# Kernel optimization log

Hardware: AMD Instinct MI355X
Metric: run time of the kernel (lower is better)

Reference implementation:

```python
import jax, jax.numpy as jnp
import numpy as np

B, T, I, O, A = 64, 512, 1024, 1024, 3


def setup_inputs() -> dict:
    key = jax.random.key(0)
    ks = jax.random.split(key, 10)
    stdv = 1.0 / np.sqrt(O)
    u = lambda k, shape: jax.random.uniform(k, shape, jnp.float32, -stdv, stdv)
    return dict(
        x=jax.random.normal(ks[0], (B, T, I), jnp.float32),
        ww_x=u(ks[1], (O, I)), ww_y=u(ks[2], (O, O)), bw=u(ks[3], (O,)),
        wb_x=u(ks[4], (O, I)), wb_y=u(ks[5], (O, O)), bb=u(ks[6], (O,)),
        wa_x=u(ks[7], (A, I)), wa_y=u(ks[8], (A, O)), ba=u(ks[9], (A,)),
    )


def _asnn_forward(x, ww_x, ww_y, bw, wb_x, wb_y, bb, wa_x, wa_y, ba):
    b_, t_, _ = x.shape
    o_ = ww_x.shape[0]
    # Precompute all input projections once (time-major for scan): [T,B,O] / [T,B,A]
    xw = jnp.einsum('bti,oi->tbo', x, ww_x) + bw
    xb = jnp.einsum('bti,oi->tbo', x, wb_x) + bb
    xa = jnp.einsum('bti,ai->tba', x, wa_x) + ba

    def step(carry, inp):
        y, h = carry  # [B,O], [B,O]
        xw_t, xb_t, xa_t = inp
        w = jax.nn.sigmoid(xw_t + h @ ww_y.T)
        b = jnp.tanh(xb_t + h @ wb_y.T)
        wa = jax.nn.sigmoid(xa_t + h @ wa_y.T)  # [B,A]
        y = w * y + b
        # original uses in-place F.leaky_relu_, so the carried y is leaky-relu'd
        y = jnp.where(y >= 0, y, 0.01 * y)
        hcat = jnp.stack([y, jnp.tanh(y), jax.nn.softplus(y)], axis=-1)  # [B,O,3]
        h = jnp.tanh(jnp.einsum('boa,ba->bo', hcat, wa) / 10.0)
        return (y, h), h

    init = (jnp.zeros((b_, o_), x.dtype), jnp.zeros((b_, o_), x.dtype))
    (y_fin, _), hs = jax.lax.scan(step, init, (xw, xb, xa))
    out = jnp.transpose(hs, (1, 0, 2))  # [B,T,O]
    return out, y_fin


def reference(x, ww_x, ww_y, bw, wb_x, wb_y, bb, wa_x, wa_y, ba):
    return _asnn_forward(x, ww_x, ww_y, bw, wb_x, wb_y, bb, wa_x, wa_y, ba)
```

## Files before the change

kernel.cpp:

```cpp
#include <hip/hip_runtime.h>
#include <hip/hip_fp16.h>


#define B_ 64
#define T_ 512
#define I_ 1024
#define O_ 1024

typedef __attribute__((ext_vector_type(8))) _Float16 half8;
typedef __attribute__((ext_vector_type(4))) float f32x4;
typedef __attribute__((ext_vector_type(4))) float float4v;
typedef __attribute__((ext_vector_type(4))) unsigned int uint4v;

__device__ __forceinline__ float sigm_f(float x) { return 1.f / (1.f + __expf(-x)); }
__device__ __forceinline__ float tanh_f(float x) { return 1.f - 2.f / (1.f + __expf(2.f * x)); }

#define WS_XW    0
#define WS_W1    134217728
#define WS_W2P   134217728
#define WS_XA    139460608
#define WS_HBUF  139853824
#define HBUF_BYTES 524288

__global__ void init_w1(const float* __restrict__ ww_x, const float* __restrict__ wb_x,
                        _Float16* __restrict__ W1) {
    const int total = 2048 * 1024;
    for (int idx = blockIdx.x * blockDim.x + threadIdx.x; idx < total;
         idx += gridDim.x * blockDim.x) {
        int n = idx >> 10, i = idx & 1023;
        float v = (n < 1024) ? ww_x[n * 1024 + i] : wb_x[(n - 1024) * 1024 + i];
        W1[idx] = (_Float16)v;
    }
}

__global__ void init_w2p(const float* __restrict__ ww_y, const float* __restrict__ wb_y,
                         const float* __restrict__ wa_y, _Float16* __restrict__ W2P) {
    const int total = 32 * 4 * 5 * 8 * 64 * 8;
    for (int idx = blockIdx.x * blockDim.x + threadIdx.x; idx < total;
         idx += gridDim.x * blockDim.x) {
        int j = idx & 7;
        int lane = (idx >> 3) & 63;
        int ktl = (idx >> 9) & 7;
        int rest = idx >> 12;
        int tile = rest % 5;
        int gw = rest / 5;
        int w = gw & 3, g = gw >> 2;
        int frow = lane & 15, fch = lane >> 4;
        int r = tile * 16 + frow;
        int k = w * 256 + ktl * 32 + fch * 8 + j;
        float v = 0.f;
        if (r < 32)      v = ww_y[(g * 32 + r) * 1024 + k];
        else if (r < 64) v = wb_y[(g * 32 + r - 32) * 1024 + k];
        else if (r < 67) v = wa_y[(r - 64) * 1024 + k];
        W2P[idx] = (_Float16)v;
    }
}

__global__ __launch_bounds__(256) void gemm1(const float* __restrict__ x,
                                             const _Float16* __restrict__ W1,
                                             const float* __restrict__ bw,
                                             const float* __restrict__ bb,
                                             _Float16* __restrict__ XW) {
    __shared__ _Float16 At[2][128][40];
    __shared__ _Float16 Bt[2][128][40];
    const int tid = threadIdx.x;
    const int lane = tid & 63, wid = tid >> 6;
    const int wr = wid >> 1, wc = wid & 1;
    const int ntile = blockIdx.x & 15;
    const int mtile = blockIdx.x >> 4;
    const long m0 = (long)mtile * 128;
    const int n0 = ntile * 128;

    const int r = tid >> 1, hf = tid & 1;
    const int bidx = (int)((m0 + r) & 63);
    const int tt = (int)((m0 + r) >> 6);
    const float* xrow = x + ((size_t)bidx * T_ + tt) * I_ + hf * 16;
    const _Float16* brow = W1 + (size_t)(n0 + r) * 1024 + hf * 16;

    float4v av[4];
    uint4v bv[2];
    auto stage_regs = [&](int kt) {
        const float4v* pa = (const float4v*)(xrow + kt * 32);
        av[0] = pa[0]; av[1] = pa[1]; av[2] = pa[2]; av[3] = pa[3];
        const uint4v* pb = (const uint4v*)(brow + kt * 32);
        bv[0] = pb[0]; bv[1] = pb[1];
    };
    auto write_lds = [&](int buf) {
        union { _Float16 h[16]; half8 v[2]; } u;
        #pragma unroll
        for (int q = 0; q < 4; ++q)
            #pragma unroll
            for (int c = 0; c < 4; ++c) u.h[q * 4 + c] = (_Float16)av[q][c];
        half8* dA = (half8*)&At[buf][r][hf * 16];
        dA[0] = u.v[0]; dA[1] = u.v[1];
        uint4v* dB = (uint4v*)&Bt[buf][r][hf * 16];
        dB[0] = bv[0]; dB[1] = bv[1];
    };

    f32x4 acc[4][4];
    #pragma unroll
    for (int i = 0; i < 4; ++i)
        #pragma unroll
        for (int j = 0; j < 4; ++j) acc[i][j] = (f32x4){0.f, 0.f, 0.f, 0.f};

    const int frow = lane & 15, fch = lane >> 4;
    auto compute = [&](int buf) {
        half8 a[4], b[4];
        #pragma unroll
        for (int i = 0; i < 4; ++i)
            a[i] = *(const half8*)&At[buf][wr * 64 + i * 16 + frow][fch * 8];
        #pragma unroll
        for (int j = 0; j < 4; ++j)
            b[j] = *(const half8*)&Bt[buf][wc * 64 + j * 16 + frow][fch * 8];
        #pragma unroll
        for (int i = 0; i < 4; ++i)
            #pragma unroll
            for (int j = 0; j < 4; ++j)
                acc[i][j] = __builtin_amdgcn_mfma_f32_16x16x32_f16(a[i], b[j], acc[i][j], 0, 0, 0);
    };

    stage_regs(0);
    write_lds(0);
    __syncthreads();
    for (int kt = 0; kt < 32; ++kt) {
        const int cur = kt & 1;
        if (kt < 31) stage_regs(kt + 1);
        compute(cur);
        if (kt < 31) { write_lds(cur ^ 1); __syncthreads(); }
    }

    const int orow = (lane >> 4) * 4, ocol = lane & 15;
    #pragma unroll
    for (int j = 0; j < 4; ++j) {
        const int n = n0 + wc * 64 + j * 16 + ocol;
        const float bias = (n < 1024) ? bw[n] : bb[n - 1024];
        #pragma unroll
        for (int i = 0; i < 4; ++i) {
            const long mb = m0 + wr * 64 + i * 16 + orow;
            #pragma unroll
            for (int rr = 0; rr < 4; ++rr)
                XW[(size_t)(mb + rr) * 2048 + n] = (_Float16)(acc[i][j][rr] + bias);
        }
    }
}

__global__ __launch_bounds__(256) void xa_proj(const float* __restrict__ x,
                                               const float* __restrict__ wa_x,
                                               const float* __restrict__ ba,
                                               float* __restrict__ XA) {
    const int wid = threadIdx.x >> 6, lane = threadIdx.x & 63;
    const long m = (long)blockIdx.x * 4 + wid;
    const int b = (int)(m & 63), t = (int)(m >> 6);
    const float4v* xr = (const float4v*)(x + ((size_t)b * T_ + t) * I_);
    const float4v* w0 = (const float4v*)(wa_x);
    const float4v* w1 = (const float4v*)(wa_x + 1024);
    const float4v* w2 = (const float4v*)(wa_x + 2048);
    float a0 = 0.f, a1 = 0.f, a2 = 0.f;
    #pragma unroll
    for (int j = 0; j < 4; ++j) {
        const int idx = j * 64 + lane;
        float4v xv = xr[idx];
        float4v v0 = w0[idx], v1 = w1[idx], v2 = w2[idx];
        a0 += xv[0] * v0[0] + xv[1] * v0[1] + xv[2] * v0[2] + xv[3] * v0[3];
        a1 += xv[0] * v1[0] + xv[1] * v1[1] + xv[2] * v1[2] + xv[3] * v1[3];
        a2 += xv[0] * v2[0] + xv[1] * v2[1] + xv[2] * v2[2] + xv[3] * v2[3];
    }
    #pragma unroll
    for (int mset = 32; mset >= 1; mset >>= 1) {
        a0 += __shfl_xor(a0, mset);
        a1 += __shfl_xor(a1, mset);
        a2 += __shfl_xor(a2, mset);
    }
    if (lane == 0) {
        XA[m * 3 + 0] = a0 + ba[0];
        XA[m * 3 + 1] = a1 + ba[1];
        XA[m * 3 + 2] = a2 + ba[2];
    }
}

#define XOR4(v) ((v[0] ^ tg) | (v[1] ^ tg) | (v[2] ^ tg) | (v[3] ^ tg))
#define PK2(lo, hi) (((lo) >> 16) | ((hi) & 0xffff0000u))
#define PACKF(dst, A, Bv) { union { unsigned u[4]; half8 h; } uu; \
    uu.u[0] = PK2(A[0], A[1]); uu.u[1] = PK2(A[2], A[3]); \
    uu.u[2] = PK2(Bv[0], Bv[1]); uu.u[3] = PK2(Bv[2], Bv[3]); dst = uu.h; }

__global__ __launch_bounds__(256, 1) void scan_kernel(
    const _Float16* __restrict__ XW, const float* __restrict__ XA,
    const _Float16* __restrict__ W2P,
    float* __restrict__ out, float* __restrict__ yfin,
    unsigned int* __restrict__ Hbuf) {
    __shared__ __align__(16) float PR[2][4][5][16][12];

    const int tid = threadIdx.x;
    const int lane = tid & 63, w = tid >> 6;
    const int d = blockIdx.x & 7, g = blockIdx.x >> 3;
    const int b0 = d * 8, n0 = g * 32;
    const int bl = tid >> 5;
    const int nn = tid & 31;
    const int frow = lane & 15, fch = lane >> 4;
    const int hi = lane >> 4, col = lane & 15;

    half8 Bf[5][8];
    {
        const _Float16* wp = W2P + ((size_t)(g * 4 + w) * 40 * 64 + lane) * 8;
        #pragma unroll
        for (int tile = 0; tile < 5; ++tile)
            #pragma unroll
            for (int ktl = 0; ktl < 8; ++ktl)
                Bf[tile][ktl] = *(const half8*)(wp + (size_t)(tile * 8 + ktl) * 512);
    }

    float y = 0.f;
    for (int t = 0; t < T_; ++t) {
        const int par = t & 1;
        f32x4 acc[5];
        #pragma unroll
        for (int tile = 0; tile < 5; ++tile) acc[tile] = (f32x4){0.f, 0.f, 0.f, 0.f};

        if (t > 0) {
            half8 af[8];
            #pragma unroll
            for (int f = 0; f < 8; ++f) af[f] = (half8)(_Float16)0.f;

            if (frow < 8) {
                const unsigned tg = (unsigned)t;
                const unsigned* hp = Hbuf + ((size_t)((t - 1) & 1) * 64 + b0 + frow) * 1024
                                     + w * 256 + fch * 8;
                uint4v q0, q1, q2, q3, q4, q5, q6, q7, q8, q9, q10, q11, q12, q13, q14, q15;
                while (true) {
                    asm volatile(
                        "global_load_dwordx4 %0, %8, off sc0 sc1\n\t"
                        "global_load_dwordx4 %1, %8, off offset:16 sc0 sc1\n\t"
                        "global_load_dwordx4 %2, %8, off offset:128 sc0 sc1\n\t"
                        "global_load_dwordx4 %3, %8, off offset:144 sc0 sc1\n\t"
                        "global_load_dwordx4 %4, %8, off offset:256 sc0 sc1\n\t"
                        "global_load_dwordx4 %5, %8, off offset:272 sc0 sc1\n\t"
                        "global_load_dwordx4 %6, %8, off offset:384 sc0 sc1\n\t"
                        "global_load_dwordx4 %7, %8, off offset:400 sc0 sc1"
                        : "=&v"(q0), "=&v"(q1), "=&v"(q2), "=&v"(q3),
                          "=&v"(q4), "=&v"(q5), "=&v"(q6), "=&v"(q7)
                        : "v"(hp) : "memory");
                    asm volatile(
                        "global_load_dwordx4 %0, %8, off offset:512 sc0 sc1\n\t"
                        "global_load_dwordx4 %1, %8, off offset:528 sc0 sc1\n\t"
                        "global_load_dwordx4 %2, %8, off offset:640 sc0 sc1\n\t"
                        "global_load_dwordx4 %3, %8, off offset:656 sc0 sc1\n\t"
                        "global_load_dwordx4 %4, %8, off offset:768 sc0 sc1\n\t"
                        "global_load_dwordx4 %5, %8, off offset:784 sc0 sc1\n\t"
                        "global_load_dwordx4 %6, %8, off offset:896 sc0 sc1\n\t"
                        "global_load_dwordx4 %7, %8, off offset:912 sc0 sc1\n\t"
                        "s_waitcnt vmcnt(0)"
                        : "=&v"(q8), "=&v"(q9), "=&v"(q10), "=&v"(q11),
                          "=&v"(q12), "=&v"(q13), "=&v"(q14), "=&v"(q15)
                        : "v"(hp) : "memory");
                    unsigned bad = (XOR4(q0) | XOR4(q1) | XOR4(q2) | XOR4(q3)
                                  | XOR4(q4) | XOR4(q5) | XOR4(q6) | XOR4(q7)
                                  | XOR4(q8) | XOR4(q9) | XOR4(q10) | XOR4(q11)
                                  | XOR4(q12) | XOR4(q13) | XOR4(q14) | XOR4(q15)) & 0xffffu;
                    if (!__any((int)bad)) break;
                }
                PACKF(af[0], q0, q1);   PACKF(af[1], q2, q3);
                PACKF(af[2], q4, q5);   PACKF(af[3], q6, q7);
                PACKF(af[4], q8, q9);   PACKF(af[5], q10, q11);
                PACKF(af[6], q12, q13); PACKF(af[7], q14, q15);
            }
            #pragma unroll
            for (int f = 0; f < 8; ++f)
                #pragma unroll
                for (int tile = 0; tile < 5; ++tile)
                    acc[tile] = __builtin_amdgcn_mfma_f32_16x16x32_f16(af[f], Bf[tile][f],
                                                                       acc[tile], 0, 0, 0);
        }

        const size_t mrow = (size_t)t * 64 + (size_t)(b0 + bl);
        const float xwv = (float)XW[mrow * 2048 + (n0 + nn)];
        const float xbv = (float)XW[mrow * 2048 + 1024 + (n0 + nn)];
        const float xa0 = XA[mrow * 3 + 0];
        const float xa1 = XA[mrow * 3 + 1];
        const float xa2 = XA[mrow * 3 + 2];

        if (t > 0 && hi < 2) {
            #pragma unroll
            for (int tile = 0; tile < 5; ++tile)
                *(f32x4*)&PR[par][w][tile][col][hi * 4] = acc[tile];
        }
        __syncthreads();

        float gw = 0.f, gb = 0.f, pav = 0.f;
        if (t > 0) {
            const int tw = nn >> 4, c = nn & 15, ac = nn & 3;
            #pragma unroll
            for (int ww = 0; ww < 4; ++ww) {
                gw += PR[par][ww][tw][c][bl];
                gb += PR[par][ww][2 + tw][c][bl];
                pav += PR[par][ww][4][ac][bl];
            }
        }
        const float pa0 = __shfl(pav, (lane & 32) + 0);
        const float pa1 = __shfl(pav, (lane & 32) + 1);
        const float pa2 = __shfl(pav, (lane & 32) + 2);

        const float wv = sigm_f(xwv + gw);
        const float bgt = tanh_f(xbv + gb);
        const float wa0 = sigm_f(xa0 + pa0);
        const float wa1 = sigm_f(xa1 + pa1);
        const float wa2 = sigm_f(xa2 + pa2);
        y = wv * y + bgt;
        y = (y >= 0.f) ? y : 0.01f * y;
        const float th = tanh_f(y);
        const float sp = (y > 20.f) ? y : __logf(1.f + __expf(y));
        const float h = tanh_f(0.1f * (y * wa0 + th * wa1 + sp * wa2));

        _Float16 hh = (_Float16)h;
        const unsigned hu = ((unsigned)*(unsigned short*)&hh << 16) | (unsigned)(t + 1);
        __hip_atomic_store(&Hbuf[((size_t)par * 64 + b0 + bl) * 1024 + n0 + nn], hu,
                           __ATOMIC_RELAXED, __HIP_MEMORY_SCOPE_AGENT);
        out[((size_t)(b0 + bl) * T_ + t) * O_ + n0 + nn] = h;
    }
    yfin[(size_t)(b0 + bl) * O_ + n0 + nn] = y;
}

extern "C" void kernel_launch(void* const* d_in, const int* in_sizes, int n_in,
                              void* d_out, int out_size, void* d_ws, size_t ws_size,
                              hipStream_t stream) {
    const float* x    = (const float*)d_in[0];
    const float* ww_x = (const float*)d_in[1];
    const float* ww_y = (const float*)d_in[2];
    const float* bw   = (const float*)d_in[3];
    const float* wb_x = (const float*)d_in[4];
    const float* wb_y = (const float*)d_in[5];
    const float* bb   = (const float*)d_in[6];
    const float* wa_x = (const float*)d_in[7];
    const float* wa_y = (const float*)d_in[8];
    const float* ba   = (const float*)d_in[9];

    char* ws = (char*)d_ws;
    _Float16* XW  = (_Float16*)(ws + WS_XW);
    _Float16* W1  = (_Float16*)(ws + WS_W1);
    _Float16* W2P = (_Float16*)(ws + WS_W2P);
    float* XA = (float*)(ws + WS_XA);
    unsigned int* Hbuf = (unsigned int*)(ws + WS_HBUF);

    float* out = (float*)d_out;
    float* yfin = out + (size_t)B_ * T_ * O_;

    hipMemsetAsync(Hbuf, 0, HBUF_BYTES, stream);
    hipLaunchKernelGGL(init_w1, dim3(2048), dim3(256), 0, stream, ww_x, wb_x, W1);
    hipLaunchKernelGGL(gemm1, dim3(4096), dim3(256), 0, stream, x, W1, bw, bb, XW);
    hipLaunchKernelGGL(init_w2p, dim3(1024), dim3(256), 0, stream, ww_y, wb_y, wa_y, W2P);
    hipLaunchKernelGGL(xa_proj, dim3(8192), dim3(256), 0, stream, x, wa_x, ba, XA);
    hipLaunchKernelGGL(scan_kernel, dim3(256), dim3(256), 0, stream,
                       XW, XA, W2P, out, yfin, Hbuf);
}
```

Before: 2.253 ms.

## Replace per-element tagged handoff with packed fp16 h buffer plus per-wave flags

The inter-block hidden-state exchange stops tagging every fp16 value with a 16-bit timestep inside a 32-bit word. h is now packed two halves per word, and each wave publishes a separate per-step flag after a vmcnt wait. Consumers spin on 128 flags for their batch group and then read half as many bytes of h. The XW/XA gate inputs for the next step are also prefetched into registers during the current step. The risks are extra flag-poll latency plus a store-then-flag ordering that depends on a waitcnt rather than a release fence.

```diff
diff --git a/kernel.cpp b/kernel.cpp
--- a/kernel.cpp
+++ b/kernel.cpp
@@ -11,16 +11,21 @@
 typedef __attribute__((ext_vector_type(4))) float f32x4;
 typedef __attribute__((ext_vector_type(4))) float float4v;
 typedef __attribute__((ext_vector_type(4))) unsigned int uint4v;
+typedef __attribute__((ext_vector_type(2))) unsigned int uint2v;
 
 __device__ __forceinline__ float sigm_f(float x) { return 1.f / (1.f + __expf(-x)); }
 __device__ __forceinline__ float tanh_f(float x) { return 1.f - 2.f / (1.f + __expf(2.f * x)); }
+__device__ __forceinline__ float h2f_bits(unsigned short u) {
+    union { unsigned short s; _Float16 h; } x; x.s = u; return (float)x.h;
+}
 
 #define WS_XW    0
 #define WS_W1    134217728
 #define WS_W2P   134217728
 #define WS_XA    139460608
 #define WS_HBUF  139853824
-#define HBUF_BYTES 524288
+#define WS_FLG   140115968
+#define FLG_BYTES 8192
 
 __global__ void init_w1(const float* __restrict__ ww_x, const float* __restrict__ wb_x,
                         _Float16* __restrict__ W1) {
@@ -178,17 +183,11 @@
     }
 }
 
-#define XOR4(v) ((v[0] ^ tg) | (v[1] ^ tg) | (v[2] ^ tg) | (v[3] ^ tg))
-#define PK2(lo, hi) (((lo) >> 16) | ((hi) & 0xffff0000u))
-#define PACKF(dst, A, Bv) { union { unsigned u[4]; half8 h; } uu; \
-    uu.u[0] = PK2(A[0], A[1]); uu.u[1] = PK2(A[2], A[3]); \
-    uu.u[2] = PK2(Bv[0], Bv[1]); uu.u[3] = PK2(Bv[2], Bv[3]); dst = uu.h; }
-
 __global__ __launch_bounds__(256, 1) void scan_kernel(
     const _Float16* __restrict__ XW, const float* __restrict__ XA,
     const _Float16* __restrict__ W2P,
     float* __restrict__ out, float* __restrict__ yfin,
-    unsigned int* __restrict__ Hbuf) {
+    unsigned int* __restrict__ Hbuf, unsigned int* __restrict__ FLG) {
     __shared__ __align__(16) float PR[2][4][5][16][12];
 
     const int tid = threadIdx.x;
@@ -209,6 +208,26 @@
             for (int ktl = 0; ktl < 8; ++ktl)
                 Bf[tile][ktl] = *(const half8*)(wp + (size_t)(tile * 8 + ktl) * 512);
     }
+    #pragma unroll
+    for (int tile = 0; tile < 5; ++tile)
+        #pragma unroll
+        for (int ktl = 0; ktl < 8; ++ktl)
+            asm volatile("" : "+v"(Bf[tile][ktl]));
+
+    uint4v aq[8];
+    #pragma unroll
+    for (int f = 0; f < 8; ++f) aq[f] = (uint4v){0u, 0u, 0u, 0u};
+
+    const unsigned short* xwp = (const unsigned short*)XW + (size_t)(b0 + bl) * 2048 + n0 + nn;
+    const unsigned short* xbp = xwp + 1024;
+    const float* xap = XA + (size_t)(b0 + bl) * 3;
+
+    unsigned short c_xw = xwp[0], c_xb = xbp[0];
+    float c_xa0 = xap[0], c_xa1 = xap[1], c_xa2 = xap[2];
+    unsigned short n_xw = 0, n_xb = 0;
+    float n_xa0 = 0.f, n_xa1 = 0.f, n_xa2 = 0.f;
+
+    const _Float16* Hh = (const _Float16*)Hbuf;
 
     float y = 0.f;
     for (int t = 0; t < T_; ++t) {
@@ -218,66 +237,44 @@
         for (int tile = 0; tile < 5; ++tile) acc[tile] = (f32x4){0.f, 0.f, 0.f, 0.f};
 
         if (t > 0) {
-            half8 af[8];
-            #pragma unroll
-            for (int f = 0; f < 8; ++f) af[f] = (half8)(_Float16)0.f;
-
+            const int parp = (t - 1) & 1;
+            {
+                const unsigned need = (unsigned)t;
+                const unsigned* fp2 = FLG + ((size_t)parp * 8 + d) * 128 + (lane << 1);
+                uint2v fv;
+                do {
+                    asm volatile("global_load_dwordx2 %0, %1, off sc0 sc1\n\t"
+                                 "s_waitcnt vmcnt(0)"
+                                 : "=v"(fv) : "v"(fp2) : "memory");
+                } while (__any((int)(fv[0] < need || fv[1] < need)));
+            }
             if (frow < 8) {
-                const unsigned tg = (unsigned)t;
-                const unsigned* hp = Hbuf + ((size_t)((t - 1) & 1) * 64 + b0 + frow) * 1024
+                const _Float16* hp = Hh + ((size_t)parp * 64 + b0 + frow) * 1024
                                      + w * 256 + fch * 8;
-                uint4v q0, q1, q2, q3, q4, q5, q6, q7, q8, q9, q10, q11, q12, q13, q14, q15;
-                while (true) {
-                    asm volatile(
-                        "global_load_dwordx4 %0, %8, off sc0 sc1\n\t"
-                        "global_load_dwordx4 %1, %8, off offset:16 sc0 sc1\n\t"
-                        "global_load_dwordx4 %2, %8, off offset:128 sc0 sc1\n\t"
-                        "global_load_dwordx4 %3, %8, off offset:144 sc0 sc1\n\t"
-                        "global_load_dwordx4 %4, %8, off offset:256 sc0 sc1\n\t"
-                        "global_load_dwordx4 %5, %8, off offset:272 sc0 sc1\n\t"
-                        "global_load_dwordx4 %6, %8, off offset:384 sc0 sc1\n\t"
-                        "global_load_dwordx4 %7, %8, off offset:400 sc0 sc1"
-                        : "=&v"(q0), "=&v"(q1), "=&v"(q2), "=&v"(q3),
-                          "=&v"(q4), "=&v"(q5), "=&v"(q6), "=&v"(q7)
-                        : "v"(hp) : "memory");
-                    asm volatile(
-                        "global_load_dwordx4 %0, %8, off offset:512 sc0 sc1\n\t"
-                        "global_load_dwordx4 %1, %8, off offset:528 sc0 sc1\n\t"
-                        "global_load_dwordx4 %2, %8, off offset:640 sc0 sc1\n\t"
-                        "global_load_dwordx4 %3, %8, off offset:656 sc0 sc1\n\t"
-                        "global_load_dwordx4 %4, %8, off offset:768 sc0 sc1\n\t"
-                        "global_load_dwordx4 %5, %8, off offset:784 sc0 sc1\n\t"
-                        "global_load_dwordx4 %6, %8, off offset:896 sc0 sc1\n\t"
-                        "global_load_dwordx4 %7, %8, off offset:912 sc0 sc1\n\t"
-                        "s_waitcnt vmcnt(0)"
-                        : "=&v"(q8), "=&v"(q9), "=&v"(q10), "=&v"(q11),
-                          "=&v"(q12), "=&v"(q13), "=&v"(q14), "=&v"(q15)
-                        : "v"(hp) : "memory");
-                    unsigned bad = (XOR4(q0) | XOR4(q1) | XOR4(q2) | XOR4(q3)
-                                  | XOR4(q4) | XOR4(q5) | XOR4(q6) | XOR4(q7)
-                                  | XOR4(q8) | XOR4(q9) | XOR4(q10) | XOR4(q11)
-                                  | XOR4(q12) | XOR4(q13) | XOR4(q14) | XOR4(q15)) & 0xffffu;
-                    if (!__any((int)bad)) break;
-                }
-                PACKF(af[0], q0, q1);   PACKF(af[1], q2, q3);
-                PACKF(af[2], q4, q5);   PACKF(af[3], q6, q7);
-                PACKF(af[4], q8, q9);   PACKF(af[5], q10, q11);
-                PACKF(af[6], q12, q13); PACKF(af[7], q14, q15);
-            }
-            #pragma unroll
-            for (int f = 0; f < 8; ++f)
+                asm volatile(
+                    "global_load_dwordx4 %0, %8, off sc0 sc1\n\t"
+                    "global_load_dwordx4 %1, %8, off offset:64 sc0 sc1\n\t"
+                    "global_load_dwordx4 %2, %8, off offset:128 sc0 sc1\n\t"
+                    "global_load_dwordx4 %3, %8, off offset:192 sc0 sc1\n\t"
+                    "global_load_dwordx4 %4, %8, off offset:256 sc0 sc1\n\t"
+                    "global_load_dwordx4 %5, %8, off offset:320 sc0 sc1\n\t"
+                    "global_load_dwordx4 %6, %8, off offset:384 sc0 sc1\n\t"
+                    "global_load_dwordx4 %7, %8, off offset:448 sc0 sc1\n\t"
+                    "s_waitcnt vmcnt(0)"
+                    : "=&v"(aq[0]), "=&v"(aq[1]), "=&v"(aq[2]), "=&v"(aq[3]),
+                      "=&v"(aq[4]), "=&v"(aq[5]), "=&v"(aq[6]), "=&v"(aq[7])
+                    : "v"(hp) : "memory");
+            }
+            #pragma unroll
+            for (int f = 0; f < 8; ++f) {
+                union { uint4v u; half8 h; } ua;
+                ua.u = aq[f];
                 #pragma unroll
                 for (int tile = 0; tile < 5; ++tile)
-                    acc[tile] = __builtin_amdgcn_mfma_f32_16x16x32_f16(af[f], Bf[tile][f],
+                    acc[tile] = __builtin_amdgcn_mfma_f32_16x16x32_f16(ua.h, Bf[tile][f],
                                                                        acc[tile], 0, 0, 0);
-        }
-
-        const size_t mrow = (size_t)t * 64 + (size_t)(b0 + bl);
-        const float xwv = (float)XW[mrow * 2048 + (n0 + nn)];
-        const float xbv = (float)XW[mrow * 2048 + 1024 + (n0 + nn)];
-        const float xa0 = XA[mrow * 3 + 0];
-        const float xa1 = XA[mrow * 3 + 1];
-        const float xa2 = XA[mrow * 3 + 2];
+            }
+        }
 
         if (t > 0 && hi < 2) {
             #pragma unroll
@@ -300,22 +297,43 @@
         const float pa1 = __shfl(pav, (lane & 32) + 1);
         const float pa2 = __shfl(pav, (lane & 32) + 2);
 
-        const float wv = sigm_f(xwv + gw);
-        const float bgt = tanh_f(xbv + gb);
-        const float wa0 = sigm_f(xa0 + pa0);
-        const float wa1 = sigm_f(xa1 + pa1);
-        const float wa2 = sigm_f(xa2 + pa2);
+        const float wv = sigm_f(h2f_bits(c_xw) + gw);
+        const float bgt = tanh_f(h2f_bits(c_xb) + gb);
+        const float wa0 = sigm_f(c_xa0 + pa0);
+        const float wa1 = sigm_f(c_xa1 + pa1);
+        const float wa2 = sigm_f(c_xa2 + pa2);
         y = wv * y + bgt;
         y = (y >= 0.f) ? y : 0.01f * y;
         const float th = tanh_f(y);
         const float sp = (y > 20.f) ? y : __logf(1.f + __expf(y));
         const float h = tanh_f(0.1f * (y * wa0 + th * wa1 + sp * wa2));
 
-        _Float16 hh = (_Float16)h;
-        const unsigned hu = ((unsigned)*(unsigned short*)&hh << 16) | (unsigned)(t + 1);
-        __hip_atomic_store(&Hbuf[((size_t)par * 64 + b0 + bl) * 1024 + n0 + nn], hu,
-                           __ATOMIC_RELAXED, __HIP_MEMORY_SCOPE_AGENT);
+        {
+            _Float16 hh = (_Float16)h;
+            union { _Float16 x; unsigned short s; } hb; hb.x = hh;
+            unsigned hu = hb.s;
+            const unsigned partner = (unsigned)__shfl_xor((int)hu, 1);
+            if (!(nn & 1)) {
+                const unsigned packed = hu | (partner << 16);
+                __hip_atomic_store(&Hbuf[(size_t)(par * 64 + b0 + bl) * 512 + ((n0 + nn) >> 1)],
+                                   packed, __ATOMIC_RELAXED, __HIP_MEMORY_SCOPE_AGENT);
+            }
+        }
+        asm volatile("s_waitcnt vmcnt(0)" ::: "memory");
+        if (lane == 0)
+            __hip_atomic_store(&FLG[((size_t)par * 8 + d) * 128 + (g << 2) + w],
+                               (unsigned)(t + 1), __ATOMIC_RELAXED, __HIP_MEMORY_SCOPE_AGENT);
+
         out[((size_t)(b0 + bl) * T_ + t) * O_ + n0 + nn] = h;
+        if (t + 1 < T_) {
+            const size_t o = (size_t)(t + 1) * 131072;
+            n_xw = xwp[o];
+            n_xb = xbp[o];
+            const float* xa = xap + (size_t)(t + 1) * 192;
+            n_xa0 = xa[0]; n_xa1 = xa[1]; n_xa2 = xa[2];
+        }
+        c_xw = n_xw; c_xb = n_xb;
+        c_xa0 = n_xa0; c_xa1 = n_xa1; c_xa2 = n_xa2;
     }
     yfin[(size_t)(b0 + bl) * O_ + n0 + nn] = y;
 }
@@ -340,15 +358,16 @@
     _Float16* W2P = (_Float16*)(ws + WS_W2P);
     float* XA = (float*)(ws + WS_XA);
     unsigned int* Hbuf = (unsigned int*)(ws + WS_HBUF);
+    unsigned int* FLG  = (unsigned int*)(ws + WS_FLG);
 
     float* out = (float*)d_out;
     float* yfin = out + (size_t)B_ * T_ * O_;
 
-    hipMemsetAsync(Hbuf, 0, HBUF_BYTES, stream);
+    hipMemsetAsync(FLG, 0, FLG_BYTES, stream);
     hipLaunchKernelGGL(init_w1, dim3(2048), dim3(256), 0, stream, ww_x, wb_x, W1);
     hipLaunchKernelGGL(gemm1, dim3(4096), dim3(256), 0, stream, x, W1, bw, bb, XW);
     hipLaunchKernelGGL(init_w2p, dim3(1024), dim3(256), 0, stream, ww_y, wb_y, wa_y, W2P);
     hipLaunchKernelGGL(xa_proj, dim3(8192), dim3(256), 0, stream, x, wa_x, ba, XA);
     hipLaunchKernelGGL(scan_kernel, dim3(256), dim3(256), 0, stream,
-                       XW, XA, W2P, out, yfin, Hbuf);
-}
+                       XW, XA, W2P, out, yfin, Hbuf, FLG);
+}
```

Measured after the change: 2.012 ms. 10.7% less time.

## Add per-group sentinel flags to scan sync and prefetch next-step inputs

Applied to the files above, without the earlier changes.

Before fetching the previous hidden state, each wave now spins on a small sentinel array holding one flag per producing wave, written after each step's h store. The old tag-checked reload of the full 16-load hidden-state slab stays in place but should normally succeed on the first pass. The per-step XW/XA input loads are software-prefetched one step ahead so their latency is off the serial path. Pack-time shifts are replaced by a byte-permute. The cost is an extra polled load and extra atomic stores per step, plus more live registers.

```diff
diff --git a/kernel.cpp b/kernel.cpp
--- a/kernel.cpp
+++ b/kernel.cpp
@@ -11,16 +11,21 @@
 typedef __attribute__((ext_vector_type(4))) float f32x4;
 typedef __attribute__((ext_vector_type(4))) float float4v;
 typedef __attribute__((ext_vector_type(4))) unsigned int uint4v;
+typedef __attribute__((ext_vector_type(2))) unsigned int uint2v;
 
 __device__ __forceinline__ float sigm_f(float x) { return 1.f / (1.f + __expf(-x)); }
 __device__ __forceinline__ float tanh_f(float x) { return 1.f - 2.f / (1.f + __expf(2.f * x)); }
+__device__ __forceinline__ float h2f_bits(unsigned short u) {
+    union { unsigned short s; _Float16 h; } x; x.s = u; return (float)x.h;
+}
 
 #define WS_XW    0
 #define WS_W1    134217728
 #define WS_W2P   134217728
 #define WS_XA    139460608
 #define WS_HBUF  139853824
-#define HBUF_BYTES 524288
+#define WS_SEN   140378112
+#define CLR_BYTES (524288 + 8192)
 
 __global__ void init_w1(const float* __restrict__ ww_x, const float* __restrict__ wb_x,
                         _Float16* __restrict__ W1) {
@@ -179,16 +184,16 @@
 }
 
 #define XOR4(v) ((v[0] ^ tg) | (v[1] ^ tg) | (v[2] ^ tg) | (v[3] ^ tg))
-#define PK2(lo, hi) (((lo) >> 16) | ((hi) & 0xffff0000u))
+#define PERM2(lo, hi) __builtin_amdgcn_perm((hi), (lo), 0x07060302u)
 #define PACKF(dst, A, Bv) { union { unsigned u[4]; half8 h; } uu; \
-    uu.u[0] = PK2(A[0], A[1]); uu.u[1] = PK2(A[2], A[3]); \
-    uu.u[2] = PK2(Bv[0], Bv[1]); uu.u[3] = PK2(Bv[2], Bv[3]); dst = uu.h; }
+    uu.u[0] = PERM2(A[0], A[1]); uu.u[1] = PERM2(A[2], A[3]); \
+    uu.u[2] = PERM2(Bv[0], Bv[1]); uu.u[3] = PERM2(Bv[2], Bv[3]); dst = uu.h; }
 
 __global__ __launch_bounds__(256, 1) void scan_kernel(
     const _Float16* __restrict__ XW, const float* __restrict__ XA,
     const _Float16* __restrict__ W2P,
     float* __restrict__ out, float* __restrict__ yfin,
-    unsigned int* __restrict__ Hbuf) {
+    unsigned int* __restrict__ Hbuf, unsigned int* __restrict__ SEN) {
     __shared__ __align__(16) float PR[2][4][5][16][12];
 
     const int tid = threadIdx.x;
@@ -209,6 +214,24 @@
             for (int ktl = 0; ktl < 8; ++ktl)
                 Bf[tile][ktl] = *(const half8*)(wp + (size_t)(tile * 8 + ktl) * 512);
     }
+    #pragma unroll
+    for (int tile = 0; tile < 5; ++tile)
+        #pragma unroll
+        for (int ktl = 0; ktl < 8; ++ktl)
+            asm volatile("" : "+v"(Bf[tile][ktl]));
+
+    uint4v q0, q1, q2, q3, q4, q5, q6, q7, q8, q9, q10, q11, q12, q13, q14, q15;
+    q0 = q1 = q2 = q3 = q4 = q5 = q6 = q7 = (uint4v){0u, 0u, 0u, 0u};
+    q8 = q9 = q10 = q11 = q12 = q13 = q14 = q15 = (uint4v){0u, 0u, 0u, 0u};
+
+    const unsigned short* xwp = (const unsigned short*)XW + (size_t)(b0 + bl) * 2048 + n0 + nn;
+    const unsigned short* xbp = xwp + 1024;
+    const float* xap = XA + (size_t)(b0 + bl) * 3;
+
+    unsigned short c_xw = xwp[0], c_xb = xbp[0];
+    float c_xa0 = xap[0], c_xa1 = xap[1], c_xa2 = xap[2];
+    unsigned short n_xw = 0, n_xb = 0;
+    float n_xa0 = 0.f, n_xa1 = 0.f, n_xa2 = 0.f;
 
     float y = 0.f;
     for (int t = 0; t < T_; ++t) {
@@ -218,15 +241,20 @@
         for (int tile = 0; tile < 5; ++tile) acc[tile] = (f32x4){0.f, 0.f, 0.f, 0.f};
 
         if (t > 0) {
-            half8 af[8];
-            #pragma unroll
-            for (int f = 0; f < 8; ++f) af[f] = (half8)(_Float16)0.f;
-
+            const int parp = (t - 1) & 1;
+            const unsigned tg = (unsigned)t;
+            {
+                const unsigned* sp = SEN + ((size_t)parp * 8 + d) * 128 + (lane << 1);
+                uint2v fv;
+                do {
+                    asm volatile("global_load_dwordx2 %0, %1, off sc0 sc1\n\t"
+                                 "s_waitcnt vmcnt(0)"
+                                 : "=v"(fv) : "v"(sp) : "memory");
+                } while (__any((int)(fv[0] < tg || fv[1] < tg)));
+            }
             if (frow < 8) {
-                const unsigned tg = (unsigned)t;
-                const unsigned* hp = Hbuf + ((size_t)((t - 1) & 1) * 64 + b0 + frow) * 1024
+                const unsigned* hp = Hbuf + ((size_t)parp * 64 + b0 + frow) * 1024
                                      + w * 256 + fch * 8;
-                uint4v q0, q1, q2, q3, q4, q5, q6, q7, q8, q9, q10, q11, q12, q13, q14, q15;
                 while (true) {
                     asm volatile(
                         "global_load_dwordx4 %0, %8, off sc0 sc1\n\t"
@@ -259,11 +287,12 @@
                                   | XOR4(q12) | XOR4(q13) | XOR4(q14) | XOR4(q15)) & 0xffffu;
                     if (!__any((int)bad)) break;
                 }
-                PACKF(af[0], q0, q1);   PACKF(af[1], q2, q3);
-                PACKF(af[2], q4, q5);   PACKF(af[3], q6, q7);
-                PACKF(af[4], q8, q9);   PACKF(af[5], q10, q11);
-                PACKF(af[6], q12, q13); PACKF(af[7], q14, q15);
             }
+            half8 af[8];
+            PACKF(af[0], q0, q1);   PACKF(af[1], q2, q3);
+            PACKF(af[2], q4, q5);   PACKF(af[3], q6, q7);
+            PACKF(af[4], q8, q9);   PACKF(af[5], q10, q11);
+            PACKF(af[6], q12, q13); PACKF(af[7], q14, q15);
             #pragma unroll
             for (int f = 0; f < 8; ++f)
                 #pragma unroll
@@ -272,12 +301,13 @@
                                                                        acc[tile], 0, 0, 0);
         }
 
-        const size_t mrow = (size_t)t * 64 + (size_t)(b0 + bl);
-        const float xwv = (float)XW[mrow * 2048 + (n0 + nn)];
-        const float xbv = (float)XW[mrow * 2048 + 1024 + (n0 + nn)];
-        const float xa0 = XA[mrow * 3 + 0];
-        const float xa1 = XA[mrow * 3 + 1];
-        const float xa2 = XA[mrow * 3 + 2];
+        if (t + 1 < T_) {
+            const size_t o = (size_t)(t + 1) * 131072;
+            n_xw = xwp[o];
+            n_xb = xbp[o];
+            const float* xa = xap + (size_t)(t + 1) * 192;
+            n_xa0 = xa[0]; n_xa1 = xa[1]; n_xa2 = xa[2];
+        }
 
         if (t > 0 && hi < 2) {
             #pragma unroll
@@ -300,22 +330,32 @@
         const float pa1 = __shfl(pav, (lane & 32) + 1);
         const float pa2 = __shfl(pav, (lane & 32) + 2);
 
-        const float wv = sigm_f(xwv + gw);
-        const float bgt = tanh_f(xbv + gb);
-        const float wa0 = sigm_f(xa0 + pa0);
-        const float wa1 = sigm_f(xa1 + pa1);
-        const float wa2 = sigm_f(xa2 + pa2);
+        const float wv = sigm_f(h2f_bits(c_xw) + gw);
+        const float bgt = tanh_f(h2f_bits(c_xb) + gb);
+        const float wa0 = sigm_f(c_xa0 + pa0);
+        const float wa1 = sigm_f(c_xa1 + pa1);
+        const float wa2 = sigm_f(c_xa2 + pa2);
         y = wv * y + bgt;
         y = (y >= 0.f) ? y : 0.01f * y;
         const float th = tanh_f(y);
         const float sp = (y > 20.f) ? y : __logf(1.f + __expf(y));
         const float h = tanh_f(0.1f * (y * wa0 + th * wa1 + sp * wa2));
 
-        _Float16 hh = (_Float16)h;
-        const unsigned hu = ((unsigned)*(unsigned short*)&hh << 16) | (unsigned)(t + 1);
-        __hip_atomic_store(&Hbuf[((size_t)par * 64 + b0 + bl) * 1024 + n0 + nn], hu,
-                           __ATOMIC_RELAXED, __HIP_MEMORY_SCOPE_AGENT);
+        {
+            _Float16 hh = (_Float16)h;
+            union { _Float16 x; unsigned short s; } hb; hb.x = hh;
+            const unsigned hu = ((unsigned)hb.s << 16) | (unsigned)(t + 1);
+            __hip_atomic_store(&Hbuf[((size_t)par * 64 + b0 + bl) * 1024 + n0 + nn], hu,
+                               __ATOMIC_RELAXED, __HIP_MEMORY_SCOPE_AGENT);
+        }
+        if (lane == 0)
+            __hip_atomic_store(&SEN[((size_t)par * 8 + d) * 128 + (g << 2) + w],
+                               (unsigned)(t + 1), __ATOMIC_RELAXED, __HIP_MEMORY_SCOPE_AGENT);
+
         out[((size_t)(b0 + bl) * T_ + t) * O_ + n0 + nn] = h;
+
+        c_xw = n_xw; c_xb = n_xb;
+        c_xa0 = n_xa0; c_xa1 = n_xa1; c_xa2 = n_xa2;
     }
     yfin[(size_t)(b0 + bl) * O_ + n0 + nn] = y;
 }
@@ -340,15 +380,16 @@
     _Float16* W2P = (_Float16*)(ws + WS_W2P);
     float* XA = (float*)(ws + WS_XA);
     unsigned int* Hbuf = (unsigned int*)(ws + WS_HBUF);
+    unsigned int* SEN  = (unsigned int*)(ws + WS_SEN);
 
     float* out = (float*)d_out;
     float* yfin = out + (size_t)B_ * T_ * O_;
 
-    hipMemsetAsync(Hbuf, 0, HBUF_BYTES, stream);
+    hipMemsetAsync(ws + WS_HBUF, 0, CLR_BYTES, stream);
     hipLaunchKernelGGL(init_w1, dim3(2048), dim3(256), 0, stream, ww_x, wb_x, W1);
     hipLaunchKernelGGL(gemm1, dim3(4096), dim3(256), 0, stream, x, W1, bw, bb, XW);
     hipLaunchKernelGGL(init_w2p, dim3(1024), dim3(256), 0, stream, ww_y, wb_y, wa_y, W2P);
     hipLaunchKernelGGL(xa_proj, dim3(8192), dim3(256), 0, stream, x, wa_x, ba, XA);
     hipLaunchKernelGGL(scan_kernel, dim3(256), dim3(256), 0, stream,
-                       XW, XA, W2P, out, yfin, Hbuf);
-}
+                       XW, XA, W2P, out, yfin, Hbuf, SEN);
+}
```

Result: slower. 4.134 ms (+83.5%).

## Replace tagged-h polling with per-wave flags, packed fp16 h, prefetch, batched output stores

Applied to the files above, without the earlier changes.

Each h value previously carried its own timestep tag, and consumers re-read the whole tagged buffer until every tag matched. Now producers write h as packed fp16 pairs, wait for the stores, then publish a per-wave flag; consumers spin on a small flag array and read h once at half the bytes. The next step's XW/XA inputs are prefetched into registers a step ahead, and the output writes are batched every 8 steps. This shortens the critical path per recurrent step, at the cost of an extra store-wait plus flag round trip, and it relies on the memory ordering of sc0 sc1 stores for correctness.

```diff
diff --git a/kernel.cpp b/kernel.cpp
--- a/kernel.cpp
+++ b/kernel.cpp
@@ -10,17 +10,24 @@
 typedef __attribute__((ext_vector_type(8))) _Float16 half8;
 typedef __attribute__((ext_vector_type(4))) float f32x4;
 typedef __attribute__((ext_vector_type(4))) float float4v;
+typedef __attribute__((ext_vector_type(2))) float float2v;
 typedef __attribute__((ext_vector_type(4))) unsigned int uint4v;
+typedef __attribute__((ext_vector_type(2))) unsigned int uint2v;
 
 __device__ __forceinline__ float sigm_f(float x) { return 1.f / (1.f + __expf(-x)); }
 __device__ __forceinline__ float tanh_f(float x) { return 1.f - 2.f / (1.f + __expf(2.f * x)); }
+__device__ __forceinline__ float h2f_bits(unsigned u) {
+    union { unsigned short s; _Float16 h; } x; x.s = (unsigned short)u; return (float)x.h;
+}
 
 #define WS_XW    0
 #define WS_W1    134217728
 #define WS_W2P   134217728
 #define WS_XA    139460608
 #define WS_HBUF  139853824
-#define HBUF_BYTES 524288
+#define WS_FLG   140116000
+#define WS_FLG_A 140116096
+#define FLG_BYTES 8192
 
 __global__ void init_w1(const float* __restrict__ ww_x, const float* __restrict__ wb_x,
                         _Float16* __restrict__ W1) {
@@ -178,17 +185,125 @@
     }
 }
 
-#define XOR4(v) ((v[0] ^ tg) | (v[1] ^ tg) | (v[2] ^ tg) | (v[3] ^ tg))
-#define PK2(lo, hi) (((lo) >> 16) | ((hi) & 0xffff0000u))
-#define PACKF(dst, A, Bv) { union { unsigned u[4]; half8 h; } uu; \
-    uu.u[0] = PK2(A[0], A[1]); uu.u[1] = PK2(A[2], A[3]); \
-    uu.u[2] = PK2(Bv[0], Bv[1]); uu.u[3] = PK2(Bv[2], Bv[3]); dst = uu.h; }
+#define STEP(T, CXW, CXB, CA01, CA2, NXW, NXB, NA01, NA2, YB) do {             \
+    const int t_ = (T);                                                        \
+    const int par_ = t_ & 1;                                                   \
+    f32x4 acc_[5];                                                             \
+    _Pragma("unroll")                                                          \
+    for (int tl = 0; tl < 5; ++tl) acc_[tl] = (f32x4){0.f, 0.f, 0.f, 0.f};     \
+    uint4v aq_[8];                                                             \
+    _Pragma("unroll")                                                          \
+    for (int f = 0; f < 8; ++f) aq_[f] = (uint4v){0u, 0u, 0u, 0u};             \
+    if (t_ > 0) {                                                              \
+        const int parp_ = (t_ - 1) & 1;                                        \
+        const unsigned tg_ = (unsigned)t_;                                     \
+                   \
+        const unsigned* fp2_ = FLG + ((size_t)parp_ * 8 + d) * 128 + (lane << 1); \
+        uint2v fv_;                                                            \
+        do {                                                                   \
+            asm volatile("global_load_dwordx2 %0, %1, off sc0 sc1\n\t"         \
+                         "s_waitcnt vmcnt(0)"                                  \
+                         : "=v"(fv_) : "v"(fp2_) : "memory");                  \
+        } while (__any((int)(fv_[0] < tg_ || fv_[1] < tg_)));                  \
+                    \
+        if (frow < 8) {                                                        \
+            const _Float16* hp_ = Hh + ((size_t)parp_ * 64 + b0 + frow) * 1024 \
+                                  + w * 256 + fch * 8;                         \
+            asm volatile(                                                      \
+                "global_load_dwordx4 %0, %8, off sc0 sc1\n\t"                  \
+                "global_load_dwordx4 %1, %8, off offset:64 sc0 sc1\n\t"        \
+                "global_load_dwordx4 %2, %8, off offset:128 sc0 sc1\n\t"       \
+                "global_load_dwordx4 %3, %8, off offset:192 sc0 sc1\n\t"       \
+                "global_load_dwordx4 %4, %8, off offset:256 sc0 sc1\n\t"       \
+                "global_load_dwordx4 %5, %8, off offset:320 sc0 sc1\n\t"       \
+                "global_load_dwordx4 %6, %8, off offset:384 sc0 sc1\n\t"       \
+                "global_load_dwordx4 %7, %8, off offset:448 sc0 sc1\n\t"       \
+                "s_waitcnt vmcnt(0)"                                           \
+                : "=&v"(aq_[0]), "=&v"(aq_[1]), "=&v"(aq_[2]), "=&v"(aq_[3]),  \
+                  "=&v"(aq_[4]), "=&v"(aq_[5]), "=&v"(aq_[6]), "=&v"(aq_[7])   \
+                : "v"(hp_) : "memory");                                        \
+        }                                                                      \
+        _Pragma("unroll")                                                      \
+        for (int f = 0; f < 8; ++f) {                                          \
+            union { uint4v u; half8 h; } ua_; ua_.u = aq_[f];                  \
+            _Pragma("unroll")                                                  \
+            for (int tl = 0; tl < 5; ++tl)                                     \
+                acc_[tl] = __builtin_amdgcn_mfma_f32_16x16x32_f16(             \
+                    ua_.h, Bf[tl][f], acc_[tl], 0, 0, 0);                      \
+        }                                                                      \
+    }                                                                          \
+         \
+    asm volatile("" : "+v"(CXW), "+v"(CXB), "+v"(CA01), "+v"(CA2));            \
+            \
+    if (t_ > 0 && hi < 2) {                                                    \
+        _Pragma("unroll")                                                      \
+        for (int tl = 0; tl < 5; ++tl)                                         \
+            *(f32x4*)&PR[par_][w][tl][col][hi * 4] = acc_[tl];                 \
+    }                                                                          \
+    __syncthreads();                                                           \
+    float gw_ = 0.f, gb_ = 0.f, pav_ = 0.f;                                    \
+    if (t_ > 0) {                                                              \
+        const int tw_ = nn >> 4, c_ = nn & 15, ac_ = nn & 3;                   \
+        _Pragma("unroll")                                                      \
+        for (int ww_ = 0; ww_ < 4; ++ww_) {                                    \
+            gw_ += PR[par_][ww_][tw_][c_][bl];                                 \
+            gb_ += PR[par_][ww_][2 + tw_][c_][bl];                             \
+            pav_ += PR[par_][ww_][4][ac_][bl];                                 \
+        }                                                                      \
+    }                                                                          \
+    const float pa0_ = __shfl(pav_, (lane & 32) + 0);                          \
+    const float pa1_ = __shfl(pav_, (lane & 32) + 1);                          \
+    const float pa2_ = __shfl(pav_, (lane & 32) + 2);                          \
+    const float wv_ = sigm_f(h2f_bits(CXW) + gw_);                             \
+    const float bgt_ = tanh_f(h2f_bits(CXB) + gb_);                            \
+    const float wa0_ = sigm_f(CA01[0] + pa0_);                                 \
+    const float wa1_ = sigm_f(CA01[1] + pa1_);                                 \
+    const float wa2_ = sigm_f(CA2 + pa2_);                                     \
+    y = wv_ * y + bgt_;                                                        \
+    y = (y >= 0.f) ? y : 0.01f * y;                                            \
+    const float th_ = tanh_f(y);                                               \
+    const float sp_ = (y > 20.f) ? y : __logf(1.f + __expf(y));                \
+    const float h_ = tanh_f(0.1f * (y * wa0_ + th_ * wa1_ + sp_ * wa2_));      \
+                      \
+    {                                                                          \
+        _Float16 hh_ = (_Float16)h_;                                           \
+        union { _Float16 x; unsigned short s; } hb_; hb_.x = hh_;              \
+        const unsigned hu_ = hb_.s;                                            \
+        const unsigned prt_ = (unsigned)__shfl_xor((int)hu_, 1);               \
+        if (!(nn & 1)) {                                                       \
+            const unsigned pk_ = hu_ | (prt_ << 16);                           \
+            unsigned* ha_ = Hbuf + ((size_t)par_ * 64 + b0 + bl) * 512         \
+                            + ((n0 + nn) >> 1);                                \
+            asm volatile("global_store_dword %0, %1, off sc0 sc1"              \
+                         :: "v"(ha_), "v"(pk_) : "memory");                    \
+        }                                                                      \
+        asm volatile("s_waitcnt vmcnt(0)" ::: "memory");                       \
+        if (lane == 0) {                                                       \
+            unsigned* fa_ = FLG + ((size_t)par_ * 8 + d) * 128 + (g << 2) + w; \
+            const unsigned fvv_ = (unsigned)(t_ + 1);                          \
+            asm volatile("global_store_dword %0, %1, off sc0 sc1"              \
+                         :: "v"(fa_), "v"(fvv_) : "memory");                   \
+        }                                                                      \
+    }                                                                          \
+    \
+    if (t_ + 1 < T_) {                                                         \
+        const unsigned short* pxw_ = xwp + (size_t)(t_ + 1) * 131072;          \
+        const float* pxa_ = xap + (size_t)(t_ + 1) * 192;                      \
+        asm volatile("global_load_ushort %0, %4, off\n\t"                      \
+                     "global_load_ushort %1, %4, off offset:2048\n\t"          \
+                     "global_load_dwordx2 %2, %5, off\n\t"                     \
+                     "global_load_dword %3, %5, off offset:8"                  \
+                     : "=&v"(NXW), "=&v"(NXB), "=&v"(NA01), "=&v"(NA2)         \
+                     : "v"(pxw_), "v"(pxa_) : "memory");                       \
+    }                                                                          \
+    YB = h_;                                                                   \
+} while (0)
 
 __global__ __launch_bounds__(256, 1) void scan_kernel(
     const _Float16* __restrict__ XW, const float* __restrict__ XA,
     const _Float16* __restrict__ W2P,
     float* __restrict__ out, float* __restrict__ yfin,
-    unsigned int* __restrict__ Hbuf) {
+    unsigned int* __restrict__ Hbuf, unsigned int* __restrict__ FLG) {
     __shared__ __align__(16) float PR[2][4][5][16][12];
 
     const int tid = threadIdx.x;
@@ -210,112 +325,39 @@
                 Bf[tile][ktl] = *(const half8*)(wp + (size_t)(tile * 8 + ktl) * 512);
     }
 
+    const _Float16* Hh = (const _Float16*)Hbuf;
+    const unsigned short* xwp = (const unsigned short*)XW + (size_t)(b0 + bl) * 2048 + n0 + nn;
+    const float* xap = XA + (size_t)(b0 + bl) * 3;
+
+    unsigned g0xw = xwp[0], g0xb = xwp[1024];
+    float2v g0a01 = (float2v){xap[0], xap[1]};
+    float g0a2 = xap[2];
+    unsigned g1xw = 0, g1xb = 0;
+    float2v g1a01 = (float2v){0.f, 0.f};
+    float g1a2 = 0.f;
+
+    float yb0, yb1, yb2, yb3, yb4, yb5, yb6, yb7;
     float y = 0.f;
-    for (int t = 0; t < T_; ++t) {
-        const int par = t & 1;
-        f32x4 acc[5];
-        #pragma unroll
-        for (int tile = 0; tile < 5; ++tile) acc[tile] = (f32x4){0.f, 0.f, 0.f, 0.f};
-
-        if (t > 0) {
-            half8 af[8];
-            #pragma unroll
-            for (int f = 0; f < 8; ++f) af[f] = (half8)(_Float16)0.f;
-
-            if (frow < 8) {
-                const unsigned tg = (unsigned)t;
-                const unsigned* hp = Hbuf + ((size_t)((t - 1) & 1) * 64 + b0 + frow) * 1024
-                                     + w * 256 + fch * 8;
-                uint4v q0, q1, q2, q3, q4, q5, q6, q7, q8, q9, q10, q11, q12, q13, q14, q15;
-                while (true) {
-                    asm volatile(
-                        "global_load_dwordx4 %0, %8, off sc0 sc1\n\t"
-                        "global_load_dwordx4 %1, %8, off offset:16 sc0 sc1\n\t"
-                        "global_load_dwordx4 %2, %8, off offset:128 sc0 sc1\n\t"
-                        "global_load_dwordx4 %3, %8, off offset:144 sc0 sc1\n\t"
-                        "global_load_dwordx4 %4, %8, off offset:256 sc0 sc1\n\t"
-                        "global_load_dwordx4 %5, %8, off offset:272 sc0 sc1\n\t"
-                        "global_load_dwordx4 %6, %8, off offset:384 sc0 sc1\n\t"
-                        "global_load_dwordx4 %7, %8, off offset:400 sc0 sc1"
-                        : "=&v"(q0), "=&v"(q1), "=&v"(q2), "=&v"(q3),
-                          "=&v"(q4), "=&v"(q5), "=&v"(q6), "=&v"(q7)
-                        : "v"(hp) : "memory");
-                    asm volatile(
-                        "global_load_dwordx4 %0, %8, off offset:512 sc0 sc1\n\t"
-                        "global_load_dwordx4 %1, %8, off offset:528 sc0 sc1\n\t"
-                        "global_load_dwordx4 %2, %8, off offset:640 sc0 sc1\n\t"
-                        "global_load_dwordx4 %3, %8, off offset:656 sc0 sc1\n\t"
-                        "global_load_dwordx4 %4, %8, off offset:768 sc0 sc1\n\t"
-                        "global_load_dwordx4 %5, %8, off offset:784 sc0 sc1\n\t"
-                        "global_load_dwordx4 %6, %8, off offset:896 sc0 sc1\n\t"
-                        "global_load_dwordx4 %7, %8, off offset:912 sc0 sc1\n\t"
-                        "s_waitcnt vmcnt(0)"
-                        : "=&v"(q8), "=&v"(q9), "=&v"(q10), "=&v"(q11),
-                          "=&v"(q12), "=&v"(q13), "=&v"(q14), "=&v"(q15)
-                        : "v"(hp) : "memory");
-                    unsigned bad = (XOR4(q0) | XOR4(q1) | XOR4(q2) | XOR4(q3)
-                                  | XOR4(q4) | XOR4(q5) | XOR4(q6) | XOR4(q7)
-                                  | XOR4(q8) | XOR4(q9) | XOR4(q10) | XOR4(q11)
-                                  | XOR4(q12) | XOR4(q13) | XOR4(q14) | XOR4(q15)) & 0xffffu;
-                    if (!__any((int)bad)) break;
-                }
-                PACKF(af[0], q0, q1);   PACKF(af[1], q2, q3);
-                PACKF(af[2], q4, q5);   PACKF(af[3], q6, q7);
-                PACKF(af[4], q8, q9);   PACKF(af[5], q10, q11);
-                PACKF(af[6], q12, q13); PACKF(af[7], q14, q15);
-            }
-            #pragma unroll
-            for (int f = 0; f < 8; ++f)
-                #pragma unroll
-                for (int tile = 0; tile < 5; ++tile)
-                    acc[tile] = __builtin_amdgcn_mfma_f32_16x16x32_f16(af[f], Bf[tile][f],
-                                                                       acc[tile], 0, 0, 0);
-        }
-
-        const size_t mrow = (size_t)t * 64 + (size_t)(b0 + bl);
-        const float xwv = (float)XW[mrow * 2048 + (n0 + nn)];
-        const float xbv = (float)XW[mrow * 2048 + 1024 + (n0 + nn)];
-        const float xa0 = XA[mrow * 3 + 0];
-        const float xa1 = XA[mrow * 3 + 1];
-        const float xa2 = XA[mrow * 3 + 2];
-
-        if (t > 0 && hi < 2) {
-            #pragma unroll
-            for (int tile = 0; tile < 5; ++tile)
-                *(f32x4*)&PR[par][w][tile][col][hi * 4] = acc[tile];
-        }
-        __syncthreads();
-
-        float gw = 0.f, gb = 0.f, pav = 0.f;
-        if (t > 0) {
-            const int tw = nn >> 4, c = nn & 15, ac = nn & 3;
-            #pragma unroll
-            for (int ww = 0; ww < 4; ++ww) {
-                gw += PR[par][ww][tw][c][bl];
-                gb += PR[par][ww][2 + tw][c][bl];
-                pav += PR[par][ww][4][ac][bl];
-            }
-        }
-        const float pa0 = __shfl(pav, (lane & 32) + 0);
-        const float pa1 = __shfl(pav, (lane & 32) + 1);
-        const float pa2 = __shfl(pav, (lane & 32) + 2);
-
-        const float wv = sigm_f(xwv + gw);
-        const float bgt = tanh_f(xbv + gb);
-        const float wa0 = sigm_f(xa0 + pa0);
-        const float wa1 = sigm_f(xa1 + pa1);
-        const float wa2 = sigm_f(xa2 + pa2);
-        y = wv * y + bgt;
-        y = (y >= 0.f) ? y : 0.01f * y;
-        const float th = tanh_f(y);
-        const float sp = (y > 20.f) ? y : __logf(1.f + __expf(y));
-        const float h = tanh_f(0.1f * (y * wa0 + th * wa1 + sp * wa2));
-
-        _Float16 hh = (_Float16)h;
-        const unsigned hu = ((unsigned)*(unsigned short*)&hh << 16) | (unsigned)(t + 1);
-        __hip_atomic_store(&Hbuf[((size_t)par * 64 + b0 + bl) * 1024 + n0 + nn], hu,
-                           __ATOMIC_RELAXED, __HIP_MEMORY_SCOPE_AGENT);
-        out[((size_t)(b0 + bl) * T_ + t) * O_ + n0 + nn] = h;
+
+    for (int t8 = 0; t8 < 64; ++t8) {
+        const int tb = t8 * 8;
+        STEP(tb + 0, g0xw, g0xb, g0a01, g0a2, g1xw, g1xb, g1a01, g1a2, yb0);
+        STEP(tb + 1, g1xw, g1xb, g1a01, g1a2, g0xw, g0xb, g0a01, g0a2, yb1);
+        STEP(tb + 2, g0xw, g0xb, g0a01, g0a2, g1xw, g1xb, g1a01, g1a2, yb2);
+        STEP(tb + 3, g1xw, g1xb, g1a01, g1a2, g0xw, g0xb, g0a01, g0a2, yb3);
+        STEP(tb + 4, g0xw, g0xb, g0a01, g0a2, g1xw, g1xb, g1a01, g1a2, yb4);
+        STEP(tb + 5, g1xw, g1xb, g1a01, g1a2, g0xw, g0xb, g0a01, g0a2, yb5);
+        STEP(tb + 6, g0xw, g0xb, g0a01, g0a2, g1xw, g1xb, g1a01, g1a2, yb6);
+        STEP(tb + 7, g1xw, g1xb, g1a01, g1a2, g0xw, g0xb, g0a01, g0a2, yb7);
+        float* ob = out + ((size_t)(b0 + bl) * T_ + tb) * O_ + n0 + nn;
+        ob[0]        = yb0;
+        ob[1 * O_]   = yb1;
+        ob[2 * O_]   = yb2;
+        ob[3 * O_]   = yb3;
+        ob[4 * O_]   = yb4;
+        ob[5 * O_]   = yb5;
+        ob[6 * O_]   = yb6;
+        ob[7 * O_]   = yb7;
     }
     yfin[(size_t)(b0 + bl) * O_ + n0 + nn] = y;
 }
@@ -340,15 +382,16 @@
     _Float16* W2P = (_Float16*)(ws + WS_W2P);
     float* XA = (float*)(ws + WS_XA);
     unsigned int* Hbuf = (unsigned int*)(ws + WS_HBUF);
+    unsigned int* FLG  = (unsigned int*)(ws + WS_FLG_A);
 
     float* out = (float*)d_out;
     float* yfin = out + (size_t)B_ * T_ * O_;
 
-    hipMemsetAsync(Hbuf, 0, HBUF_BYTES, stream);
+    hipMemsetAsync(ws + WS_FLG_A, 0, FLG_BYTES, stream);
     hipLaunchKernelGGL(init_w1, dim3(2048), dim3(256), 0, stream, ww_x, wb_x, W1);
     hipLaunchKernelGGL(gemm1, dim3(4096), dim3(256), 0, stream, x, W1, bw, bb, XW);
     hipLaunchKernelGGL(init_w2p, dim3(1024), dim3(256), 0, stream, ww_y, wb_y, wa_y, W2P);
     hipLaunchKernelGGL(xa_proj, dim3(8192), dim3(256), 0, stream, x, wa_x, ba, XA);
     hipLaunchKernelGGL(scan_kernel, dim3(256), dim3(256), 0, stream,
-                       XW, XA, W2P, out, yfin, Hbuf);
-}
+                       XW, XA, W2P, out, yfin, Hbuf, FLG);
+}
```

After: 4.266 ms. +89.4%, slower.
